# Kernel optimization log

Hardware: AMD Instinct MI355X
Metric: run time of the kernel (lower is better)

Reference implementation:

```python
import math
from itertools import combinations
import jax, jax.numpy as jnp
import numpy as np

B, N, KR, KA, T = 16, 96, 16, 8, 4
RCR, RCA = 5.2, 3.5


def setup_inputs() -> dict:
    key = jax.random.key(0)
    k1, k2 = jax.random.split(key)
    coords = jax.random.normal(k1, (B, N, 3), dtype=jnp.float32) * 3.0
    atom_types = jax.random.randint(k2, (N,), 0, T)
    EtaR = jnp.full((T, KR), 16.0, dtype=jnp.float32)
    ShfR = jnp.tile(jnp.linspace(0.9, 5.0, KR, dtype=jnp.float32), (T, 1))
    Zeta = jnp.full((T, KA), 32.0, dtype=jnp.float32)
    EtaA = jnp.tile(jnp.linspace(0.5, 8.0, KA, dtype=jnp.float32), (T, 1))
    return {"coords": coords, "atom_types": atom_types,
            "EtaR": EtaR, "ShfR": ShfR, "Zeta": Zeta, "EtaA": EtaA}


def _pairwise_vector(coords):
    # coords: [B, N, 3] -> rij: [B, N, N-1, 3] (diagonal removed, same order as masked_select)
    n = coords.shape[1]
    idx = np.array([[j for j in range(n) if j != i] for i in range(n)])  # [N, N-1]
    rij = coords[:, :, None, :] - coords[:, None, :, :]                   # [B, N, N, 3]
    return rij[:, np.arange(n)[:, None], idx]                             # [B, N, N-1, 3]


def reference(coords, atom_types, EtaR, ShfR, Zeta, EtaA):
    rij = _pairwise_vector(coords)                 # [B, N, N-1, 3]
    er = EtaR[atom_types]                          # [N, KR]
    sr = ShfR[atom_types]                          # [N, KR]
    ze = Zeta[atom_types]                          # [N, KA]
    ea = EtaA[atom_types]                          # [N, KA]

    # ---- G2 (radial) ----
    dij = jnp.linalg.norm(rij, axis=3)             # [B, N, N-1]
    fij = (jnp.cos(dij / RCR * math.pi) + 1) * 0.5
    g2 = jnp.sum(jnp.exp(-er[:, None, :] * (dij[..., None] - sr[:, None, :]) ** 2)
                 * fij[..., None], axis=2)         # [B, N, KR]

    # ---- G3 (angular) ----
    n1 = rij.shape[2]
    c = np.array(list(combinations(range(n1), 2)))  # [P, 2]
    rp = rij[:, :, c]                               # [B, N, P, 2, 3]
    r12, r13 = rp[:, :, :, 0], rp[:, :, :, 1]
    r23 = r12 - r13
    d12 = jnp.linalg.norm(r12, axis=3)              # [B, N, P]
    d13 = jnp.linalg.norm(r13, axis=3)
    d23 = jnp.linalg.norm(r23, axis=3)
    f12 = (jnp.cos(d12 / RCA * math.pi) + 1) * 0.5
    f13 = (jnp.cos(d13 / RCA * math.pi) + 1) * 0.5
    f23 = (jnp.cos(d23 / RCA * math.pi) + 1) * 0.5
    cosine = jnp.einsum('bnpk,bnpk->bnp', r12, r13) / (d12 * d13)
    g3 = jnp.sum(2.0 ** (1 - ze[:, None, :])
                 * (1 + cosine[..., None]) ** ze[:, None, :]
                 * jnp.exp(-ea[:, None, :] * (d12 ** 2 + d13 ** 2 + d23 ** 2)[..., None])
                 * (f12 * f13 * f23)[..., None], axis=2)  # [B, N, KA]

    return jnp.concatenate((g2, g3), axis=2)        # [B, N, KR+KA]
```

## Files before the change

### kernel.cpp

```cpp
#include <hip/hip_runtime.h>

namespace {
constexpr int Bc  = 16;
constexpr int Nc  = 96;
constexpr int KRc = 16;
constexpr int KAc = 8;
constexpr int NOUT = KRc + KAc;
constexpr int NNb  = Nc - 1;
constexpr int PADN = 144;
constexpr float RCRf = 5.2f;
constexpr float RCAf = 3.5f;
constexpr float L2E  = 1.4426950408889634f;
}

typedef float v2f __attribute__((ext_vector_type(2)));
typedef float v4f __attribute__((ext_vector_type(4)));

__device__ __forceinline__ v2f sp(float x) { return (v2f){x, x}; }
__device__ __forceinline__ v2f pfma(v2f a, v2f b, v2f c) {
    return __builtin_elementwise_fma(a, b, c);
}
__device__ __forceinline__ v2f pmax(v2f a, v2f b) {
    return __builtin_elementwise_max(a, b);
}
__device__ __forceinline__ v2f pexp2(v2f x) {
    return (v2f){__builtin_amdgcn_exp2f(x.x), __builtin_amdgcn_exp2f(x.y)};
}
__device__ __forceinline__ v2f pcosr(v2f rev) {
    return (v2f){__builtin_amdgcn_cosf(__builtin_amdgcn_fractf(rev.x)),
                 __builtin_amdgcn_cosf(__builtin_amdgcn_fractf(rev.y))};
}
__device__ __forceinline__ v2f psqrt(v2f x) {
    return (v2f){__builtin_amdgcn_sqrtf(x.x), __builtin_amdgcn_sqrtf(x.y)};
}
__device__ __forceinline__ float cos_rev(float rev) {
    return __builtin_amdgcn_cosf(__builtin_amdgcn_fractf(rev));
}

__global__ __launch_bounds__(256, 6) void ani_feat_kernel(
    const float* __restrict__ coords,
    const int*   __restrict__ atom_types,
    const float* __restrict__ EtaR,
    const float* __restrict__ ShfR,
    const float* __restrict__ Zeta,
    const float* __restrict__ EtaA,
    float* __restrict__ out)
{
    const int bi = blockIdx.x;
    const int b  = bi / Nc;
    const int i  = bi - b * Nc;
    const int t  = threadIdx.x;

    __shared__ float4 su[NNb];
    __shared__ float  ufa[NNb], sfr[NNb];
    __shared__ v4f  pxy[PADN];
    __shared__ v4f  pzd[PADN];
    __shared__ v2f  pfa[PADN];
    __shared__ float pr[16][KRc];
    __shared__ float red[4][KAc];

    const int ti = atom_types[i];

    if (t < NNb) {
        const float* cb = coords + (size_t)(b * Nc) * 3;
        int j = t + (t >= i);
        float dx = cb[i*3+0] - cb[j*3+0];
        float dy = cb[i*3+1] - cb[j*3+1];
        float dz = cb[i*3+2] - cb[j*3+2];
        float d2 = dx*dx + dy*dy + dz*dz;
        float d  = __builtin_amdgcn_sqrtf(d2);
        float inv = __builtin_amdgcn_rcpf(d);
        su[t]  = make_float4(dx*inv, dy*inv, dz*inv, d);
        ufa[t] = fmaf(cos_rev(d * (0.5f / RCAf)), 0.5f, 0.5f);
        sfr[t] = fmaf(cos_rev(d * (0.5f / RCRf)), 0.5f, 0.5f);
    }

    bool fast;
    float ea0, dLs, c10;
    {
        float z0 = Zeta[ti * KAc + 0];
        bool zu = true;
#pragma unroll
        for (int k = 1; k < KAc; ++k) zu = zu && (Zeta[ti * KAc + k] == z0);
        float e0v = EtaA[ti * KAc + 0] * L2E;
        float e1v = EtaA[ti * KAc + 1] * L2E;
        float dv  = e1v - e0v;
        bool ar = true;
#pragma unroll
        for (int k = 2; k < KAc; ++k) {
            float ev = EtaA[ti * KAc + k] * L2E;
            ar = ar && (fabsf(ev - (e0v + dv * (float)k)) <=
                        1e-5f * fabsf(ev) + 1e-7f);
        }
        fast = zu && ar && (z0 == 32.0f);
        ea0 = e0v; dLs = dv; c10 = 1.0f - z0;
    }

    __syncthreads();

    if (t < NNb) {
        int s1 = t + 1; if (s1 >= NNb) s1 = 0;
        float4 a = su[t], c = su[s1];
        pxy[t] = (v4f){a.x, c.x, a.y, c.y};
        pzd[t] = (v4f){a.z, c.z, a.w, c.w};
        pfa[t] = (v2f){ufa[t], ufa[s1]};
    }
    if (t < PADN - NNb) {
        int s1 = t + 1;
        float4 a = su[t], c = su[s1];
        pxy[NNb + t] = (v4f){a.x, c.x, a.y, c.y};
        pzd[NNb + t] = (v4f){a.z, c.z, a.w, c.w};
        pfa[NNb + t] = (v2f){ufa[t], ufa[s1]};
    }

    {
        const int k = t & 15, g2 = t >> 4;
        float er  = EtaR[ti * KRc + k];
        float sr  = ShfR[ti * KRc + k];
        float erL = -er * L2E;
        float acc = 0.0f;
        for (int jj = g2; jj < NNb; jj += 16) {
            float dd = su[jj].w - sr;
            acc += __builtin_amdgcn_exp2f(erL * dd * dd) * sfr[jj];
        }
        pr[g2][k] = acc;
    }
    __syncthreads();

    const bool act = (t < 2 * NNb);
    const int  g   = (t >= NNb) ? 1 : 0;
    const int  j   = act ? (t - g * NNb) : 0;
    const float4 A  = su[j];
    const float faj = act ? ufa[j] : 0.0f;
    const float d2A  = A.w * A.w;
    const float m2Aw = -2.0f * A.w;
    const int   j2b  = j + (g ? 25 : 1);

    float av[KAc];

    if (fast) {
        v2f acc2[KAc];
#pragma unroll
        for (int k = 0; k < KAc; ++k) acc2[k] = sp(0.0f);

        if (act) {
            const v2f fajv  = sp(faj);
            const v2f lastm = g ? (v2f){faj, 0.0f} : fajv;

#define ANG_IT(IT, FAJV)                                                    \
            {                                                               \
                v4f xy = pxy[j2b + 2 * (IT)];                               \
                v4f zd = pzd[j2b + 2 * (IT)];                               \
                v2f fb = pfa[j2b + 2 * (IT)];                               \
                v2f Bx = xy.xy, By = xy.zw;                                 \
                v2f Bz = zd.xy, Bw = zd.zw;                                 \
                v2f cosv = pfma(sp(A.x), Bx, pfma(sp(A.y), By, sp(A.z)*Bz));\
                v2f sAB  = pfma(Bw, Bw, sp(d2A));                           \
                v2f d23sq = pmax(pfma(sp(m2Aw)*Bw, cosv, sAB), sp(0.0f));   \
                v2f f23 = pfma(pcosr(psqrt(d23sq) * sp(0.5f/RCAf)),         \
                               sp(0.5f), sp(0.5f));                         \
                v2f fprod = (FAJV) * fb * f23;                              \
                v2f s  = sAB + d23sq;                                       \
                v2f tt = pmax(sp(1.0f) + cosv, sp(0.0f));                   \
                v2f t2 = tt*tt, t4 = t2*t2, t8 = t4*t4, t16 = t8*t8;        \
                v2f F  = t16 * t16 * fprod;                                 \
                v2f e0 = pexp2(pfma(sp(-ea0), s, sp(c10)));                 \
                v2f q  = pexp2(sp(-dLs) * s);                               \
                v2f q2 = q * q;                                             \
                v2f e1 = e0*q,  e2 = e0*q2, e3 = e1*q2;                     \
                v2f e4 = e2*q2, e5 = e3*q2, e6 = e4*q2, e7 = e5*q2;         \
                acc2[0] = pfma(F, e0, acc2[0]);                             \
                acc2[1] = pfma(F, e1, acc2[1]);                             \
                acc2[2] = pfma(F, e2, acc2[2]);                             \
                acc2[3] = pfma(F, e3, acc2[3]);                             \
                acc2[4] = pfma(F, e4, acc2[4]);                             \
                acc2[5] = pfma(F, e5, acc2[5]);                             \
                acc2[6] = pfma(F, e6, acc2[6]);                             \
                acc2[7] = pfma(F, e7, acc2[7]);                             \
            }

            ANG_IT(0, fajv)  ANG_IT(1, fajv)  ANG_IT(2, fajv)
            ANG_IT(3, fajv)  ANG_IT(4, fajv)  ANG_IT(5, fajv)
            ANG_IT(6, fajv)  ANG_IT(7, fajv)  ANG_IT(8, fajv)
            ANG_IT(9, fajv)  ANG_IT(10, fajv) ANG_IT(11, lastm)
#undef ANG_IT
        }
#pragma unroll
        for (int k = 0; k < KAc; ++k) av[k] = acc2[k].x + acc2[k].y;
    } else {
        float zek[KAc], c1k[KAc], eaL[KAc];
#pragma unroll
        for (int k = 0; k < KAc; ++k) {
            float z = Zeta[ti * KAc + k];
            zek[k] = z;
            c1k[k] = 1.0f - z;
            eaL[k] = EtaA[ti * KAc + k] * L2E;
        }
        float accS[KAc];
#pragma unroll
        for (int k = 0; k < KAc; ++k) accS[k] = 0.0f;

        if (act) {
            for (int r = 0; r < 24; ++r) {
                int rr = (g ? 25 : 1) + r;
                float lv = (rr <= 47) ? 1.0f : 0.0f;
                int j2 = j + rr; if (j2 >= NNb) j2 -= NNb;
                float4 Bq = su[j2];
                float fb = ufa[j2];
                float cosv = fmaf(A.x, Bq.x, fmaf(A.y, Bq.y, A.z * Bq.z));
                float sAB  = fmaf(Bq.w, Bq.w, d2A);
                float d23sq = fmaxf(fmaf(m2Aw * Bq.w, cosv, sAB), 0.0f);
                float d23 = __builtin_amdgcn_sqrtf(d23sq);
                float f23 = fmaf(cos_rev(d23 * (0.5f / RCAf)), 0.5f, 0.5f);
                float fprod = faj * fb * f23 * lv;
                float s  = sAB + d23sq;
                float tt = fmaxf(1.0f + cosv, 0.0f);
                float l2 = __builtin_amdgcn_logf(tt);
#pragma unroll
                for (int k = 0; k < KAc; ++k) {
                    float E = fmaf(zek[k], l2, c1k[k]);
                    E = fmaf(-eaL[k], s, E);
                    accS[k] += __builtin_amdgcn_exp2f(E) * fprod;
                }
            }
        }
#pragma unroll
        for (int k = 0; k < KAc; ++k) av[k] = accS[k];
    }

    const int lane = t & 63, wv = t >> 6;
#pragma unroll
    for (int k = 0; k < KAc; ++k) {
        float v = av[k];
#pragma unroll
        for (int off = 32; off; off >>= 1) v += __shfl_xor(v, off, 64);
        if (lane == 0) red[wv][k] = v;
    }
    __syncthreads();

    if (t < KAc) {
        out[bi * NOUT + KRc + t] =
            red[0][t] + red[1][t] + red[2][t] + red[3][t];
    }
    if (t < KRc) {
        float s = 0.0f;
#pragma unroll
        for (int g2 = 0; g2 < 16; ++g2) s += pr[g2][t];
        out[bi * NOUT + t] = s;
    }
}

extern "C" void kernel_launch(void* const* d_in, const int* in_sizes, int n_in,
                              void* d_out, int out_size, void* d_ws, size_t ws_size,
                              hipStream_t stream) {
    const float* coords     = (const float*)d_in[0];
    const int*   atom_types = (const int*)d_in[1];
    const float* EtaR       = (const float*)d_in[2];
    const float* ShfR       = (const float*)d_in[3];
    const float* Zeta       = (const float*)d_in[4];
    const float* EtaA       = (const float*)d_in[5];
    float* out = (float*)d_out;

    ani_feat_kernel<<<dim3(Bc * Nc), dim3(256), 0, stream>>>(
        coords, atom_types, EtaR, ShfR, Zeta, EtaA, out);
}
```

Before: 16.77 us.

## Split angular work of tail atoms across two blocks to balance the wave tail

The grid grows from 1536 to 2048 blocks. The first 1024 atoms keep one block each, and each of the remaining 512 atoms is split across two blocks that each compute half of the angular iterations. Angular results are combined with atomicAdd into an output that a preceding memset clears, and only the primary block writes the radial part. The launch-bounds occupancy hint is raised from 6 to 8. The intent is to fill a second partial wave of blocks more evenly, at the cost of an extra memset, atomics, and redundant shared-memory setup in the split blocks.

Measured after the change: 23.85 us. 1.42x slower.

```diff
diff --git a/kernel.cpp b/kernel.cpp
--- a/kernel.cpp
+++ b/kernel.cpp
@@ -8,6 +8,7 @@
 constexpr int NOUT = KRc + KAc;
 constexpr int NNb  = Nc - 1;
 constexpr int PADN = 144;
+constexpr int NFULL = 1024;
 constexpr float RCRf = 5.2f;
 constexpr float RCAf = 3.5f;
 constexpr float L2E  = 1.4426950408889634f;
@@ -37,7 +38,7 @@
     return __builtin_amdgcn_cosf(__builtin_amdgcn_fractf(rev));
 }
 
-__global__ __launch_bounds__(256, 6) void ani_feat_kernel(
+__global__ __launch_bounds__(256, 8) void ani_feat_kernel(
     const float* __restrict__ coords,
     const int*   __restrict__ atom_types,
     const float* __restrict__ EtaR,
@@ -46,7 +47,12 @@
     const float* __restrict__ EtaA,
     float* __restrict__ out)
 {
-    const int bi = blockIdx.x;
+    const int blk = blockIdx.x;
+    const bool split = (blk >= NFULL);
+    const int  gma   = split ? (blk - NFULL) : 0;
+    const int  bi    = split ? (NFULL + (gma >> 1)) : blk;
+    const int  half  = split ? (gma & 1) : 0;
+    const bool primary = !split || (half == 0);
     const int b  = bi / Nc;
     const int i  = bi - b * Nc;
     const int t  = threadIdx.x;
@@ -113,7 +119,7 @@
         pfa[NNb + t] = (v2f){ufa[t], ufa[s1]};
     }
 
-    {
+    if (primary) {
         const int k = t & 15, g2 = t >> 4;
         float er  = EtaR[ti * KRc + k];
         float sr  = ShfR[ti * KRc + k];
@@ -134,7 +140,8 @@
     const float faj = act ? ufa[j] : 0.0f;
     const float d2A  = A.w * A.w;
     const float m2Aw = -2.0f * A.w;
-    const int   j2b  = j + (g ? 25 : 1);
+    const int   itbase = split ? 6 * half : 0;
+    const int   j2b  = j + (g ? 25 : 1) + 2 * itbase;
 
     float av[KAc];
 
@@ -145,7 +152,7 @@
 
         if (act) {
             const v2f fajv  = sp(faj);
-            const v2f lastm = g ? (v2f){faj, 0.0f} : fajv;
+            const v2f tailm = g ? (v2f){faj, 0.0f} : fajv;
 
 #define ANG_IT(IT, FAJV)                                                    \
             {                                                               \
@@ -179,10 +186,16 @@
                 acc2[7] = pfma(F, e7, acc2[7]);                             \
             }
 
-            ANG_IT(0, fajv)  ANG_IT(1, fajv)  ANG_IT(2, fajv)
-            ANG_IT(3, fajv)  ANG_IT(4, fajv)  ANG_IT(5, fajv)
-            ANG_IT(6, fajv)  ANG_IT(7, fajv)  ANG_IT(8, fajv)
-            ANG_IT(9, fajv)  ANG_IT(10, fajv) ANG_IT(11, lastm)
+            if (!split) {
+                ANG_IT(0, fajv)  ANG_IT(1, fajv)  ANG_IT(2, fajv)
+                ANG_IT(3, fajv)  ANG_IT(4, fajv)  ANG_IT(5, fajv)
+                ANG_IT(6, fajv)  ANG_IT(7, fajv)  ANG_IT(8, fajv)
+                ANG_IT(9, fajv)  ANG_IT(10, fajv) ANG_IT(11, tailm)
+            } else {
+                const v2f last6 = half ? tailm : fajv;
+                ANG_IT(0, fajv)  ANG_IT(1, fajv)  ANG_IT(2, fajv)
+                ANG_IT(3, fajv)  ANG_IT(4, fajv)  ANG_IT(5, last6)
+            }
 #undef ANG_IT
         }
 #pragma unroll
@@ -201,10 +214,13 @@
         for (int k = 0; k < KAc; ++k) accS[k] = 0.0f;
 
         if (act) {
-            for (int r = 0; r < 24; ++r) {
-                int rr = (g ? 25 : 1) + r;
+            const int nr = split ? 12 : 24;
+            int j2 = j + (g ? 25 : 1) + 2 * itbase;
+            while (j2 >= NNb) j2 -= NNb;
+            for (int r = 0; r < nr; ++r) {
+                int rg = 2 * itbase + r;
+                int rr = (g ? 25 : 1) + rg;
                 float lv = (rr <= 47) ? 1.0f : 0.0f;
-                int j2 = j + rr; if (j2 >= NNb) j2 -= NNb;
                 float4 Bq = su[j2];
                 float fb = ufa[j2];
                 float cosv = fmaf(A.x, Bq.x, fmaf(A.y, Bq.y, A.z * Bq.z));
@@ -222,6 +238,7 @@
                     E = fmaf(-eaL[k], s, E);
                     accS[k] += __builtin_amdgcn_exp2f(E) * fprod;
                 }
+                ++j2; if (j2 >= NNb) j2 = 0;
             }
         }
 #pragma unroll
@@ -239,10 +256,10 @@
     __syncthreads();
 
     if (t < KAc) {
-        out[bi * NOUT + KRc + t] =
-            red[0][t] + red[1][t] + red[2][t] + red[3][t];
-    }
-    if (t < KRc) {
+        float v = red[0][t] + red[1][t] + red[2][t] + red[3][t];
+        atomicAdd(&out[bi * NOUT + KRc + t], v);
+    }
+    if (primary && t < KRc) {
         float s = 0.0f;
 #pragma unroll
         for (int g2 = 0; g2 < 16; ++g2) s += pr[g2][t];
@@ -261,6 +278,7 @@
     const float* EtaA       = (const float*)d_in[5];
     float* out = (float*)d_out;
 
-    ani_feat_kernel<<<dim3(Bc * Nc), dim3(256), 0, stream>>>(
+    hipMemsetAsync(out, 0, (size_t)out_size * sizeof(float), stream);
+    ani_feat_kernel<<<dim3(2048), dim3(256), 0, stream>>>(
         coords, atom_types, EtaR, ShfR, Zeta, EtaA, out);
 }
```

## Compact neighbors by Gaussian cutoff and distribute angular pairs over all threads

Applied to the files above, without the earlier changes.

Neighbors whose squared distance exceeds a threshold where the smallest angular Gaussian decays below float relevance are filtered out with ballot and popcount into a compacted shared list. The angular pair loop then enumerates only pairs of surviving neighbors, mapped flat across all 256 threads. The radial loop also uses the compact list when every radial term is provably negligible beyond the threshold. The change trims exp and cosine work for distant pairs and drops the packed v2f layout. In exchange it adds an extra barrier, an index decode per pair, and a dependence on how many neighbors survive.

Result: faster. 15.87 us (-5.3%).

```diff
diff --git a/kernel.cpp b/kernel.cpp
--- a/kernel.cpp
+++ b/kernel.cpp
@@ -7,34 +7,16 @@
 constexpr int KAc = 8;
 constexpr int NOUT = KRc + KAc;
 constexpr int NNb  = Nc - 1;
-constexpr int PADN = 144;
 constexpr float RCRf = 5.2f;
 constexpr float RCAf = 3.5f;
 constexpr float L2E  = 1.4426950408889634f;
 }
 
-typedef float v2f __attribute__((ext_vector_type(2)));
-typedef float v4f __attribute__((ext_vector_type(4)));
-
-__device__ __forceinline__ v2f sp(float x) { return (v2f){x, x}; }
-__device__ __forceinline__ v2f pfma(v2f a, v2f b, v2f c) {
-    return __builtin_elementwise_fma(a, b, c);
-}
-__device__ __forceinline__ v2f pmax(v2f a, v2f b) {
-    return __builtin_elementwise_max(a, b);
-}
-__device__ __forceinline__ v2f pexp2(v2f x) {
-    return (v2f){__builtin_amdgcn_exp2f(x.x), __builtin_amdgcn_exp2f(x.y)};
-}
-__device__ __forceinline__ v2f pcosr(v2f rev) {
-    return (v2f){__builtin_amdgcn_cosf(__builtin_amdgcn_fractf(rev.x)),
-                 __builtin_amdgcn_cosf(__builtin_amdgcn_fractf(rev.y))};
-}
-__device__ __forceinline__ v2f psqrt(v2f x) {
-    return (v2f){__builtin_amdgcn_sqrtf(x.x), __builtin_amdgcn_sqrtf(x.y)};
-}
 __device__ __forceinline__ float cos_rev(float rev) {
     return __builtin_amdgcn_cosf(__builtin_amdgcn_fractf(rev));
+}
+__device__ __forceinline__ float exp2g(float x) {
+    return __builtin_amdgcn_exp2f(x);
 }
 
 __global__ __launch_bounds__(256, 6) void ani_feat_kernel(
@@ -50,17 +32,43 @@
     const int b  = bi / Nc;
     const int i  = bi - b * Nc;
     const int t  = threadIdx.x;
+    const int lane = t & 63, wv = t >> 6;
 
     __shared__ float4 su[NNb];
     __shared__ float  ufa[NNb], sfr[NNb];
-    __shared__ v4f  pxy[PADN];
-    __shared__ v4f  pzd[PADN];
-    __shared__ v2f  pfa[PADN];
-    __shared__ float pr[16][KRc];
-    __shared__ float red[4][KAc];
+    __shared__ float4 ca4[NNb];
+    __shared__ float  cfa[NNb], cfr[NNb];
+    __shared__ float  pr[16][KRc];
+    __shared__ float  red[4][KAc];
+    __shared__ int    sM[2];
 
     const int ti = atom_types[i];
 
+    bool fast;
+    float ea0, dLs, c10, THR;
+    {
+        float z0 = Zeta[ti * KAc + 0];
+        bool zu = true;
+#pragma unroll
+        for (int k = 1; k < KAc; ++k) zu = zu && (Zeta[ti * KAc + k] == z0);
+        ea0 = EtaA[ti * KAc + 0] * L2E;
+        float e1v = EtaA[ti * KAc + 1] * L2E;
+        dLs = e1v - ea0;
+        bool ar = true;
+#pragma unroll
+        for (int k = 2; k < KAc; ++k) {
+            float ev = EtaA[ti * KAc + k] * L2E;
+            ar = ar && (fabsf(ev - (ea0 + dLs * (float)k)) <=
+                        1e-5f * fabsf(ev) + 1e-7f);
+        }
+        float eamin = fminf(ea0, ea0 + 7.0f * dLs);
+        fast = zu && ar && (z0 == 32.0f) && (eamin > 1e-6f);
+        THR  = fast ? (26.0f / eamin) : 1e30f;
+        c10  = 1.0f - z0;
+    }
+
+    float st_ux = 0, st_uy = 0, st_uz = 0, st_d = 0, st_fa = 0, st_fr = 0;
+    bool pred = false;
     if (t < NNb) {
         const float* cb = coords + (size_t)(b * Nc) * 3;
         int j = t + (t >= i);
@@ -70,123 +78,125 @@
         float d2 = dx*dx + dy*dy + dz*dz;
         float d  = __builtin_amdgcn_sqrtf(d2);
         float inv = __builtin_amdgcn_rcpf(d);
-        su[t]  = make_float4(dx*inv, dy*inv, dz*inv, d);
-        ufa[t] = fmaf(cos_rev(d * (0.5f / RCAf)), 0.5f, 0.5f);
-        sfr[t] = fmaf(cos_rev(d * (0.5f / RCRf)), 0.5f, 0.5f);
-    }
-
-    bool fast;
-    float ea0, dLs, c10;
-    {
-        float z0 = Zeta[ti * KAc + 0];
-        bool zu = true;
-#pragma unroll
-        for (int k = 1; k < KAc; ++k) zu = zu && (Zeta[ti * KAc + k] == z0);
-        float e0v = EtaA[ti * KAc + 0] * L2E;
-        float e1v = EtaA[ti * KAc + 1] * L2E;
-        float dv  = e1v - e0v;
-        bool ar = true;
-#pragma unroll
-        for (int k = 2; k < KAc; ++k) {
-            float ev = EtaA[ti * KAc + k] * L2E;
-            ar = ar && (fabsf(ev - (e0v + dv * (float)k)) <=
-                        1e-5f * fabsf(ev) + 1e-7f);
-        }
-        fast = zu && ar && (z0 == 32.0f);
-        ea0 = e0v; dLs = dv; c10 = 1.0f - z0;
-    }
-
+        st_ux = dx*inv; st_uy = dy*inv; st_uz = dz*inv; st_d = d;
+        st_fa = fmaf(cos_rev(d * (0.5f / RCAf)), 0.5f, 0.5f);
+        st_fr = fmaf(cos_rev(d * (0.5f / RCRf)), 0.5f, 0.5f);
+        su[t]  = make_float4(st_ux, st_uy, st_uz, d);
+        ufa[t] = st_fa;
+        sfr[t] = st_fr;
+        pred = (d2 <= THR);
+    }
+    unsigned long long mask = __ballot(pred);
+    unsigned long long ltm  = (1ull << lane) - 1ull;
+    if (wv == 0) {
+        int pos = (int)__popcll(mask & ltm);
+        if (pred) {
+            ca4[pos] = make_float4(st_ux, st_uy, st_uz, st_d);
+            cfa[pos] = st_fa; cfr[pos] = st_fr;
+        }
+        if (t == 0) sM[0] = (int)__popcll(mask);
+    }
     __syncthreads();
 
-    if (t < NNb) {
-        int s1 = t + 1; if (s1 >= NNb) s1 = 0;
-        float4 a = su[t], c = su[s1];
-        pxy[t] = (v4f){a.x, c.x, a.y, c.y};
-        pzd[t] = (v4f){a.z, c.z, a.w, c.w};
-        pfa[t] = (v2f){ufa[t], ufa[s1]};
-    }
-    if (t < PADN - NNb) {
-        int s1 = t + 1;
-        float4 a = su[t], c = su[s1];
-        pxy[NNb + t] = (v4f){a.x, c.x, a.y, c.y};
-        pzd[NNb + t] = (v4f){a.z, c.z, a.w, c.w};
-        pfa[NNb + t] = (v2f){ufa[t], ufa[s1]};
-    }
+    if (wv == 1) {
+        int base = sM[0];
+        int pos = base + (int)__popcll(mask & ltm);
+        if (pred) {
+            ca4[pos] = make_float4(st_ux, st_uy, st_uz, st_d);
+            cfa[pos] = st_fa; cfr[pos] = st_fr;
+        }
+        if (lane == 0) sM[1] = base + (int)__popcll(mask);
+    }
+    __syncthreads();
+
+    const int M = sM[1];
 
     {
         const int k = t & 15, g2 = t >> 4;
         float er  = EtaR[ti * KRc + k];
         float sr  = ShfR[ti * KRc + k];
+        float sqT = __builtin_amdgcn_sqrtf(THR);
+        bool okk = (sr < sqT) && (er * (sqT - sr) * (sqT - sr) >= 16.0f);
+        bool okr = __all(okk) && fast;
         float erL = -er * L2E;
         float acc = 0.0f;
-        for (int jj = g2; jj < NNb; jj += 16) {
-            float dd = su[jj].w - sr;
-            acc += __builtin_amdgcn_exp2f(erL * dd * dd) * sfr[jj];
+        if (okr) {
+            for (int jj = g2; jj < M; jj += 16) {
+                float dd = ca4[jj].w - sr;
+                acc += exp2g(erL * dd * dd) * cfr[jj];
+            }
+        } else {
+            for (int jj = g2; jj < NNb; jj += 16) {
+                float dd = su[jj].w - sr;
+                acc += exp2g(erL * dd * dd) * sfr[jj];
+            }
         }
         pr[g2][k] = acc;
     }
-    __syncthreads();
-
-    const bool act = (t < 2 * NNb);
-    const int  g   = (t >= NNb) ? 1 : 0;
-    const int  j   = act ? (t - g * NNb) : 0;
-    const float4 A  = su[j];
-    const float faj = act ? ufa[j] : 0.0f;
-    const float d2A  = A.w * A.w;
-    const float m2Aw = -2.0f * A.w;
-    const int   j2b  = j + (g ? 25 : 1);
 
     float av[KAc];
 
     if (fast) {
-        v2f acc2[KAc];
-#pragma unroll
-        for (int k = 0; k < KAc; ++k) acc2[k] = sp(0.0f);
-
-        if (act) {
-            const v2f fajv  = sp(faj);
-            const v2f lastm = g ? (v2f){faj, 0.0f} : fajv;
-
-#define ANG_IT(IT, FAJV)                                                    \
-            {                                                               \
-                v4f xy = pxy[j2b + 2 * (IT)];                               \
-                v4f zd = pzd[j2b + 2 * (IT)];                               \
-                v2f fb = pfa[j2b + 2 * (IT)];                               \
-                v2f Bx = xy.xy, By = xy.zw;                                 \
-                v2f Bz = zd.xy, Bw = zd.zw;                                 \
-                v2f cosv = pfma(sp(A.x), Bx, pfma(sp(A.y), By, sp(A.z)*Bz));\
-                v2f sAB  = pfma(Bw, Bw, sp(d2A));                           \
-                v2f d23sq = pmax(pfma(sp(m2Aw)*Bw, cosv, sAB), sp(0.0f));   \
-                v2f f23 = pfma(pcosr(psqrt(d23sq) * sp(0.5f/RCAf)),         \
-                               sp(0.5f), sp(0.5f));                         \
-                v2f fprod = (FAJV) * fb * f23;                              \
-                v2f s  = sAB + d23sq;                                       \
-                v2f tt = pmax(sp(1.0f) + cosv, sp(0.0f));                   \
-                v2f t2 = tt*tt, t4 = t2*t2, t8 = t4*t4, t16 = t8*t8;        \
-                v2f F  = t16 * t16 * fprod;                                 \
-                v2f e0 = pexp2(pfma(sp(-ea0), s, sp(c10)));                 \
-                v2f q  = pexp2(sp(-dLs) * s);                               \
-                v2f q2 = q * q;                                             \
-                v2f e1 = e0*q,  e2 = e0*q2, e3 = e1*q2;                     \
-                v2f e4 = e2*q2, e5 = e3*q2, e6 = e4*q2, e7 = e5*q2;         \
-                acc2[0] = pfma(F, e0, acc2[0]);                             \
-                acc2[1] = pfma(F, e1, acc2[1]);                             \
-                acc2[2] = pfma(F, e2, acc2[2]);                             \
-                acc2[3] = pfma(F, e3, acc2[3]);                             \
-                acc2[4] = pfma(F, e4, acc2[4]);                             \
-                acc2[5] = pfma(F, e5, acc2[5]);                             \
-                acc2[6] = pfma(F, e6, acc2[6]);                             \
-                acc2[7] = pfma(F, e7, acc2[7]);                             \
-            }
-
-            ANG_IT(0, fajv)  ANG_IT(1, fajv)  ANG_IT(2, fajv)
-            ANG_IT(3, fajv)  ANG_IT(4, fajv)  ANG_IT(5, fajv)
-            ANG_IT(6, fajv)  ANG_IT(7, fajv)  ANG_IT(8, fajv)
-            ANG_IT(9, fajv)  ANG_IT(10, fajv) ANG_IT(11, lastm)
-#undef ANG_IT
-        }
-#pragma unroll
-        for (int k = 0; k < KAc; ++k) av[k] = acc2[k].x + acc2[k].y;
+        float acc[KAc];
+#pragma unroll
+        for (int k = 0; k < KAc; ++k) acc[k] = 0.0f;
+
+        const int K      = (M - 1) >> 1;
+        const int fullS  = M * K;
+        const int tailS  = (M & 1) ? 0 : (M >> 1);
+        const int nps    = fullS + tailS;
+        const int rounds = (nps + 255) >> 8;
+        const float invM = 1.0f / (float)M;
+
+        for (int r = 0; r < rounds; ++r) {
+            int slot = (r << 8) + t;
+            bool valid = slot < nps;
+            int a, rr;
+            if (slot < fullS) {
+                int rp = (int)((float)slot * invM);
+                a = slot - rp * M;
+                if (a < 0)       { --rp; a += M; }
+                else if (a >= M) { ++rp; a -= M; }
+                rr = rp + 1;
+            } else {
+                a  = slot - fullS;
+                rr = M >> 1;
+            }
+            if (!valid) { a = 0; rr = 0; }
+            int bq = a + rr; if (bq >= M) bq -= M;
+
+            float4 A  = ca4[a];
+            float4 Bv = ca4[bq];
+            float faa = cfa[a], fab = cfa[bq];
+            float da = A.w, db = Bv.w;
+            float cosv = fmaf(A.x, Bv.x, fmaf(A.y, Bv.y, A.z * Bv.z));
+            float sAB  = fmaf(da, da, db * db);
+            float d23sq = fmaxf(fmaf(-2.0f * da * db, cosv, sAB), 0.0f);
+            float f23 = fmaf(cos_rev(__builtin_amdgcn_sqrtf(d23sq) *
+                                     (0.5f / RCAf)), 0.5f, 0.5f);
+            float fprod = faa * fab * f23;
+            float s  = sAB + d23sq;
+            float tt = 1.0f + cosv;
+            float t2 = tt*tt, t4 = t2*t2, t8 = t4*t4, t16 = t8*t8;
+            float F  = t16 * t16 * fprod;
+            F = valid ? F : 0.0f;
+            float e0 = exp2g(-ea0 * s);
+            float q  = exp2g(-dLs * s);
+            float q2 = q * q;
+            float e1 = e0*q,  e2 = e0*q2, e3 = e1*q2;
+            float e4 = e2*q2, e5 = e3*q2, e6 = e4*q2, e7 = e5*q2;
+            acc[0] = fmaf(F, e0, acc[0]);
+            acc[1] = fmaf(F, e1, acc[1]);
+            acc[2] = fmaf(F, e2, acc[2]);
+            acc[3] = fmaf(F, e3, acc[3]);
+            acc[4] = fmaf(F, e4, acc[4]);
+            acc[5] = fmaf(F, e5, acc[5]);
+            acc[6] = fmaf(F, e6, acc[6]);
+            acc[7] = fmaf(F, e7, acc[7]);
+        }
+        const float p21z = exp2g(c10);
+#pragma unroll
+        for (int k = 0; k < KAc; ++k) av[k] = acc[k] * p21z;
     } else {
         float zek[KAc], c1k[KAc], eaL[KAc];
 #pragma unroll
@@ -200,7 +210,14 @@
 #pragma unroll
         for (int k = 0; k < KAc; ++k) accS[k] = 0.0f;
 
+        const bool act = (t < 2 * NNb);
+        const int  g   = (t >= NNb) ? 1 : 0;
+        const int  j   = act ? (t - g * NNb) : 0;
         if (act) {
+            float4 A = su[j];
+            float faj = ufa[j];
+            float d2A = A.w * A.w;
+            float m2Aw = -2.0f * A.w;
             for (int r = 0; r < 24; ++r) {
                 int rr = (g ? 25 : 1) + r;
                 float lv = (rr <= 47) ? 1.0f : 0.0f;
@@ -220,7 +237,7 @@
                 for (int k = 0; k < KAc; ++k) {
                     float E = fmaf(zek[k], l2, c1k[k]);
                     E = fmaf(-eaL[k], s, E);
-                    accS[k] += __builtin_amdgcn_exp2f(E) * fprod;
+                    accS[k] += exp2g(E) * fprod;
                 }
             }
         }
@@ -228,7 +245,6 @@
         for (int k = 0; k < KAc; ++k) av[k] = accS[k];
     }
 
-    const int lane = t & 63, wv = t >> 6;
 #pragma unroll
     for (int k = 0; k < KAc; ++k) {
         float v = av[k];
```
